# Optimization experiments

Measured on AMD Instinct MI355X. Metric: run time of the kernel, lower is better.

## Reference

```python
import jax, jax.numpy as jnp
import numpy as np

N = 32768          # total nodes
B = 64             # number of graphs (batch.max()+1)
IN_C = 256
OUT_C = 256
NUM_SCALES = 4
NUM_HEADS = 8
BN_EPS = 1e-5


def setup_inputs() -> dict:
    key = jax.random.key(0)
    ks = jax.random.split(key, 10)
    out_s = OUT_C // NUM_SCALES
    x = jax.random.normal(ks[0], (N, IN_C), jnp.float32)
    spectral = jax.random.normal(ks[1], (NUM_SCALES, N, IN_C), jnp.float32)
    batch = jnp.sort(jax.random.randint(ks[2], (N,), 0, B)).astype(jnp.int64)
    # per-scale Linear weights (glorot) and zero biases; stored as [S, in, out_s]
    g = (6.0 / (IN_C + out_s)) ** 0.5
    Ws = jax.random.uniform(ks[3], (NUM_SCALES, IN_C, out_s), jnp.float32, -g, g)
    bs = jnp.zeros((NUM_SCALES, out_s), jnp.float32)
    # MultiheadAttention params (torch layout: in_proj [3E,E], out_proj [E,E])
    s_in = (1.0 / OUT_C) ** 0.5
    W_in = jax.random.uniform(ks[4], (3 * OUT_C, OUT_C), jnp.float32, -s_in, s_in)
    b_in = jnp.zeros((3 * OUT_C,), jnp.float32)
    W_out = jax.random.uniform(ks[5], (OUT_C, OUT_C), jnp.float32, -s_in, s_in)
    b_out = jnp.zeros((OUT_C,), jnp.float32)
    gamma = jnp.ones((OUT_C,), jnp.float32)
    beta = jnp.zeros((OUT_C,), jnp.float32)
    return {"x": x, "spectral": spectral, "Ws": Ws, "bs": bs,
            "W_in": W_in, "b_in": b_in, "W_out": W_out, "b_out": b_out,
            "gamma": gamma, "beta": beta, "batch": batch}


def _forward(x, spectral, Ws, bs, W_in, b_in, W_out, b_out, gamma, beta, batch):
    n, E = x.shape[0], W_out.shape[0]
    # per-scale linear on (x + spectral_feat), concat over scales -> [N, E]
    scale_out = jnp.einsum('sni,sio->sno', x[None] + spectral, Ws) + bs[:, None, :]
    h = jnp.moveaxis(scale_out, 0, 1).reshape(n, E)
    # ragged -> dense padding (batch is sorted segment ids)
    counts = jnp.bincount(batch, length=B)
    max_nodes = int(np.asarray(counts).max())  # data-dependent pad, as in torch
    starts = jnp.concatenate([jnp.zeros((1,), counts.dtype), jnp.cumsum(counts)[:-1]])
    pos = jnp.arange(n) - starts[batch]
    h_pad = jnp.zeros((B, max_nodes, E), h.dtype).at[batch, pos].set(h)
    # MHA over padded graphs (no key-padding mask, matching the source)
    hd = E // NUM_HEADS
    qkv = h_pad @ W_in.T + b_in                       # [B, M, 3E]
    q, k, v = jnp.split(qkv, 3, axis=-1)
    def heads(t):
        return t.reshape(B, max_nodes, NUM_HEADS, hd).transpose(0, 2, 1, 3)
    q, k, v = heads(q) * (hd ** -0.5), heads(k), heads(v)
    attn = jax.nn.softmax(jnp.einsum('bhqd,bhkd->bhqk', q, k), axis=-1)
    ctx = jnp.einsum('bhqk,bhkd->bhqd', attn, v)
    ctx = ctx.transpose(0, 2, 1, 3).reshape(B, max_nodes, E)
    h_att = ctx @ W_out.T + b_out
    # dense -> ragged unpad
    h2 = h_att[batch, pos]                            # [N, E]
    # BatchNorm1d (training-mode batch stats, deterministic) + ReLU; dropout=eval
    mean = h2.mean(axis=0)
    var = h2.var(axis=0)
    hn = (h2 - mean) * jax.lax.rsqrt(var + BN_EPS) * gamma + beta
    return jax.nn.relu(hn)


def reference(x, spectral, Ws, bs, W_in, b_in, W_out, b_out, gamma, beta, batch):
    return _forward(x, spectral, Ws, bs, W_in, b_in, W_out, b_out, gamma, beta, batch)
```

## Files before the change

kernel.cpp:

```cpp
#include <hip/hip_runtime.h>


typedef __attribute__((ext_vector_type(8))) short frag8;
typedef __attribute__((ext_vector_type(4))) float f32x4;
typedef __attribute__((ext_vector_type(8))) unsigned short ushort8;

#define NN 32768
#define NB 64
#define CIN 256
#define COUT 256
#define NHEAD 8
#define HD 32

#define BM 128
#define BK 64
#define LDK 72
#define KT 128

__device__ inline unsigned short f2bf(float f) {
  unsigned u = __builtin_bit_cast(unsigned, f);
  u += 0x7FFFu + ((u >> 16) & 1u);
  return (unsigned short)(u >> 16);
}
__device__ inline unsigned pack2bf(float a, float b) {
  return (unsigned)f2bf(a) | ((unsigned)f2bf(b) << 16);
}

__global__ void k_bounds(const int* __restrict__ batch, int* __restrict__ meta) {
  int i = blockIdx.x * 256 + threadIdx.x;
  if (i >= NN) return;
  int v = batch[i];
  int prev = (i == 0) ? -1 : batch[i - 1];
  for (int bb = prev + 1; bb <= v; ++bb) meta[NB + bb] = i;
}
__global__ void k_meta2(int* __restrict__ meta) {
  __shared__ int mx[NB];
  int b = threadIdx.x;
  int s = meta[NB + b];
  int e = (b == 63) ? NN : meta[NB + b + 1];
  meta[b] = e - s;
  mx[b] = e - s;
  __syncthreads();
  if (b == 0) {
    int m = 0;
    for (int j = 0; j < NB; ++j) m = max(m, mx[j]);
    meta[2 * NB] = m;
  }
}

__global__ void k_prep(const float* __restrict__ Ws, const float* __restrict__ Win,
                       const float* __restrict__ Wout,
                       unsigned short* __restrict__ wst, unsigned short* __restrict__ winb,
                       unsigned short* __restrict__ woutb) {
  int tid = blockIdx.x * 256 + threadIdx.x;
  if (tid < 4 * 64 * 256) {
    int s = tid >> 14, rem = tid & 16383, o = rem >> 8, i = rem & 255;
    wst[tid] = f2bf(Ws[((s * 256) + i) * 64 + o]);
  } else if (tid < 4 * 64 * 256 + 768 * 256) {
    int t2 = tid - 4 * 64 * 256;
    winb[t2] = f2bf(Win[t2]);
  } else if (tid < 4 * 64 * 256 + 768 * 256 + 256 * 256) {
    int t3 = tid - (4 * 64 * 256 + 768 * 256);
    woutb[t3] = f2bf(Wout[t3]);
  }
}

template <int NT>
__device__ inline void mfma_tile(const unsigned short (*As)[LDK],
                                 const unsigned short (*Bs)[LDK],
                                 f32x4 acc[2][NT], int wave, int lane) {
  int m16 = lane & 15, quad = lane >> 4;
#pragma unroll
  for (int kk = 0; kk < 2; ++kk) {
    frag8 a[2], b[NT];
#pragma unroll
    for (int mi = 0; mi < 2; ++mi)
      a[mi] = *(const frag8*)&As[wave * 32 + mi * 16 + m16][kk * 32 + quad * 8];
#pragma unroll
    for (int ni = 0; ni < NT; ++ni)
      b[ni] = *(const frag8*)&Bs[ni * 16 + m16][kk * 32 + quad * 8];
#pragma unroll
    for (int mi = 0; mi < 2; ++mi)
#pragma unroll
      for (int ni = 0; ni < NT; ++ni)
        acc[mi][ni] = __builtin_amdgcn_mfma_f32_16x16x32_bf16(a[mi], b[ni], acc[mi][ni], 0, 0, 0);
  }
}

__device__ inline void stage_B64(const unsigned short* __restrict__ Wt, int c0, int k0,
                                 unsigned short (*Bs)[LDK], int t) {
  int n = t & 63, seg = t >> 6;
  const unsigned short* src = Wt + (size_t)(c0 + n) * 256 + k0 + seg * 16;
  uint4 v0 = *(const uint4*)src;
  uint4 v1 = *(const uint4*)(src + 8);
  *(uint4*)&Bs[n][seg * 16] = v0;
  *(uint4*)&Bs[n][seg * 16 + 8] = v1;
}

__device__ inline void stage_B128(const unsigned short* __restrict__ Wt, int c0, int k0,
                                  unsigned short (*Bs)[LDK], int t) {
  int n = t >> 1, half = t & 1;
  const unsigned short* src = Wt + (size_t)(c0 + n) * 256 + k0 + half * 32;
#pragma unroll
  for (int i = 0; i < 4; ++i) {
    uint4 v = *(const uint4*)(src + i * 8);
    *(uint4*)&Bs[n][half * 32 + i * 8] = v;
  }
}

__device__ inline void stage_A_bf(const unsigned short* __restrict__ A, int lda, int r0, int k0,
                                  unsigned short (*As)[LDK], int t) {
  int r = t >> 1, half = t & 1;
  const unsigned short* src = A + (size_t)(r0 + r) * lda + k0 + half * 32;
#pragma unroll
  for (int i = 0; i < 4; ++i) {
    uint4 v = *(const uint4*)(src + i * 8);
    *(uint4*)&As[r][half * 32 + i * 8] = v;
  }
}

__global__ __launch_bounds__(256) void k_scale(const float* __restrict__ x,
                                               const float* __restrict__ spec,
                                               const unsigned short* __restrict__ wst,
                                               const float* __restrict__ bs,
                                               unsigned short* __restrict__ h) {
  __shared__ unsigned short As[BM][LDK];
  __shared__ unsigned short Bs[64][LDK];
  int t = threadIdx.x, lane = t & 63, wave = t >> 6;
  int r0 = blockIdx.x * BM, s = blockIdx.y;
  f32x4 z = {0.f, 0.f, 0.f, 0.f};
  f32x4 acc[2][4];
#pragma unroll
  for (int mi = 0; mi < 2; ++mi)
#pragma unroll
    for (int ni = 0; ni < 4; ++ni) acc[mi][ni] = z;

  const float* sb = spec + (size_t)s * NN * CIN;
  for (int k0 = 0; k0 < CIN; k0 += BK) {
    {
      int r = t >> 1, half = t & 1;
      const float* xs = x + (size_t)(r0 + r) * CIN + k0 + half * 32;
      const float* ss = sb + (size_t)(r0 + r) * CIN + k0 + half * 32;
#pragma unroll
      for (int i = 0; i < 8; ++i) {
        float4 xv = *(const float4*)(xs + i * 4);
        float4 sv = *(const float4*)(ss + i * 4);
        ushort4 o;
        o.x = f2bf(xv.x + sv.x); o.y = f2bf(xv.y + sv.y);
        o.z = f2bf(xv.z + sv.z); o.w = f2bf(xv.w + sv.w);
        *(ushort4*)&As[r][half * 32 + i * 4] = o;
      }
    }
    stage_B64(wst + (size_t)s * 64 * 256, 0, k0, Bs, t);
    __syncthreads();
    mfma_tile<4>(As, Bs, acc, wave, lane);
    __syncthreads();
  }
  int m16 = lane & 15, quad = lane >> 4;
#pragma unroll
  for (int mi = 0; mi < 2; ++mi)
#pragma unroll
    for (int ni = 0; ni < 4; ++ni) {
      int col = ni * 16 + m16;
      float bias = bs[s * 64 + col];
#pragma unroll
      for (int r = 0; r < 4; ++r) {
        int row = r0 + wave * 32 + mi * 16 + quad * 4 + r;
        h[(size_t)row * COUT + s * 64 + col] = f2bf(acc[mi][ni][r] + bias);
      }
    }
}

template <int LDOUT, bool F32OUT, bool STATS>
__global__ __launch_bounds__(256) void k_lin(const unsigned short* __restrict__ A,
                                             const unsigned short* __restrict__ Wt,
                                             const float* __restrict__ bias,
                                             void* __restrict__ out,
                                             float* __restrict__ sums) {
  __shared__ unsigned short As[BM][LDK];
  __shared__ unsigned short Bs[128][LDK];
  int t = threadIdx.x, lane = t & 63, wave = t >> 6;
  int r0 = blockIdx.x * BM, c0 = blockIdx.y * 128;
  f32x4 z = {0.f, 0.f, 0.f, 0.f};
  f32x4 acc[2][8];
#pragma unroll
  for (int mi = 0; mi < 2; ++mi)
#pragma unroll
    for (int ni = 0; ni < 8; ++ni) acc[mi][ni] = z;

  for (int k0 = 0; k0 < 256; k0 += BK) {
    stage_A_bf(A, 256, r0, k0, As, t);
    stage_B128(Wt, c0, k0, Bs, t);
    __syncthreads();
    mfma_tile<8>(As, Bs, acc, wave, lane);
    __syncthreads();
  }
  int m16 = lane & 15, quad = lane >> 4;
  float cs[8], cs2[8];
#pragma unroll
  for (int ni = 0; ni < 8; ++ni) { cs[ni] = 0.f; cs2[ni] = 0.f; }
#pragma unroll
  for (int mi = 0; mi < 2; ++mi)
#pragma unroll
    for (int ni = 0; ni < 8; ++ni) {
      int col = c0 + ni * 16 + m16;
      float bv = bias[col];
#pragma unroll
      for (int r = 0; r < 4; ++r) {
        int row = r0 + wave * 32 + mi * 16 + quad * 4 + r;
        float v = acc[mi][ni][r] + bv;
        if constexpr (STATS) { cs[ni] += v; cs2[ni] += v * v; }
        if constexpr (F32OUT)
          ((float*)out)[(size_t)row * LDOUT + col] = v;
        else
          ((unsigned short*)out)[(size_t)row * LDOUT + col] = f2bf(v);
      }
    }
  if constexpr (STATS) {
#pragma unroll
    for (int ni = 0; ni < 8; ++ni) {
      float a = cs[ni], b2 = cs2[ni];
      a += __shfl_xor(a, 16); a += __shfl_xor(a, 32);
      b2 += __shfl_xor(b2, 16); b2 += __shfl_xor(b2, 32);
      if (quad == 0) {
        atomicAdd(&sums[c0 + ni * 16 + m16], a);
        atomicAdd(&sums[256 + c0 + ni * 16 + m16], b2);
      }
    }
  }
}

__global__ __launch_bounds__(256) void k_attn_mfma(const unsigned short* __restrict__ qkv,
                                                   const int* __restrict__ meta,
                                                   unsigned short* __restrict__ ctx) {
  int b = blockIdx.x >> 3, head = blockIdx.x & 7;
  int c = meta[b], st = meta[NB + b], M = meta[2 * NB];
  int q0 = blockIdx.y * 128;
  if (q0 >= c) return;

  __shared__ unsigned short Vt[32][KT + 8];

  int t = threadIdx.x, lane = t & 63, wave = t >> 6;
  int m16 = lane & 15, quad = lane >> 4;
  const float SCALE = 0.17677669529663687f;
  float extra = (float)(M - c);

  int qbase = q0 + wave * 32;
  frag8 qf[2];
#pragma unroll
  for (int qg = 0; qg < 2; ++qg) {
    int qrow = qbase + qg * 16 + m16;
    qf[qg] = *(const frag8*)(qkv + (size_t)(st + qrow) * 768 + head * 32 + quad * 8);
  }

  f32x4 zz = {0.f, 0.f, 0.f, 0.f};
  f32x4 O[2][2];
  float lp[2] = {0.f, 0.f};
#pragma unroll
  for (int qg = 0; qg < 2; ++qg) { O[qg][0] = zz; O[qg][1] = zz; }

  int sl0 = m16 + ((quad & 1) << 5);
  int sl1 = sl0 + 16;

  for (int kt = 0; kt < c; kt += KT) {
    {
      int key = t >> 1, dh0 = (t & 1) * 16;
      const unsigned short* vp = qkv + (size_t)(st + kt + key) * 768 + 512 + head * 32 + dh0;
      ushort8 v0 = *(const ushort8*)vp;
      ushort8 v1 = *(const ushort8*)(vp + 8);
#pragma unroll
      for (int i = 0; i < 8; ++i) {
        Vt[dh0 + i][key] = v0[i];
        Vt[dh0 + 8 + i][key] = v1[i];
      }
    }
    __syncthreads();

#pragma unroll
    for (int sub = 0; sub < 4; ++sub) {
      int ks = kt + sub * 32;
      frag8 kf[2];
#pragma unroll
      for (int kh = 0; kh < 2; ++kh) {
        int krow = ks + kh * 16 + m16;
        kf[kh] = *(const frag8*)(qkv + (size_t)(st + krow) * 768 + 256 + head * 32 + quad * 8);
      }
      unsigned pk[2][2][2];
#pragma unroll
      for (int qg = 0; qg < 2; ++qg)
#pragma unroll
        for (int kh = 0; kh < 2; ++kh) {
          f32x4 s = __builtin_amdgcn_mfma_f32_16x16x32_bf16(kf[kh], qf[qg], zz, 0, 0, 0);
          float p[4];
#pragma unroll
          for (int r = 0; r < 4; ++r) {
            int key = ks + kh * 16 + quad * 4 + r;
            float msk = (key < c) ? 1.f : 0.f;
            p[r] = msk * __expf(s[r] * SCALE);
            lp[qg] += p[r];
          }
          pk[qg][kh][0] = pack2bf(p[0], p[1]);
          pk[qg][kh][1] = pack2bf(p[2], p[3]);
        }
      frag8 vf[2];
#pragma unroll
      for (int dh = 0; dh < 2; ++dh)
        vf[dh] = *(const frag8*)&Vt[dh * 16 + m16][sub * 32 + quad * 8];
#pragma unroll
      for (int qg = 0; qg < 2; ++qg) {
        unsigned a0 = __shfl(pk[qg][0][0], sl0), a1 = __shfl(pk[qg][0][1], sl0);
        unsigned a2 = __shfl(pk[qg][0][0], sl1), a3 = __shfl(pk[qg][0][1], sl1);
        unsigned b0 = __shfl(pk[qg][1][0], sl0), b1 = __shfl(pk[qg][1][1], sl0);
        unsigned b2 = __shfl(pk[qg][1][0], sl1), b3 = __shfl(pk[qg][1][1], sl1);
        uint4 pw;
        pw.x = (quad < 2) ? a0 : b0;
        pw.y = (quad < 2) ? a1 : b1;
        pw.z = (quad < 2) ? a2 : b2;
        pw.w = (quad < 2) ? a3 : b3;
        frag8 pf = __builtin_bit_cast(frag8, pw);
#pragma unroll
        for (int dh = 0; dh < 2; ++dh)
          O[qg][dh] = __builtin_amdgcn_mfma_f32_16x16x32_bf16(pf, vf[dh], O[qg][dh], 0, 0, 0);
      }
    }
    __syncthreads();
  }

#pragma unroll
  for (int qg = 0; qg < 2; ++qg) {
    float v = lp[qg];
    v += __shfl_xor(v, 16);
    v += __shfl_xor(v, 32);
    lp[qg] = v;
  }

#pragma unroll
  for (int qg = 0; qg < 2; ++qg)
#pragma unroll
    for (int r = 0; r < 4; ++r) {
      int qrow = qbase + qg * 16 + quad * 4 + r;
      float lsum = __shfl(lp[qg], quad * 4 + r);
      if (qrow < c) {
        float inv = 1.f / (lsum + extra);
        unsigned short* op = ctx + (size_t)(st + qrow) * 256 + head * 32;
        op[m16] = f2bf(O[qg][0][r] * inv);
        op[16 + m16] = f2bf(O[qg][1][r] * inv);
      }
    }
}

__global__ void k_bn_final(const float* __restrict__ sums, const float* __restrict__ gamma,
                           const float* __restrict__ beta, float* __restrict__ bnp) {
  int c = threadIdx.x;
  float mean = sums[c] * (1.0f / NN);
  float var = sums[256 + c] * (1.0f / NN) - mean * mean;
  float sc = rsqrtf(var + 1e-5f) * gamma[c];
  bnp[c] = sc;
  bnp[256 + c] = beta[c] - mean * sc;
}

__global__ __launch_bounds__(256) void k_bn_apply(const float* __restrict__ h,
                                                  const float* __restrict__ bnp,
                                                  float* __restrict__ out) {
  size_t i4 = (size_t)blockIdx.x * 256 + threadIdx.x;
  float4 v = *(const float4*)(h + i4 * 4);
  int c = (int)((i4 * 4) & 255);
  float4 sc = *(const float4*)(bnp + c);
  float4 sh = *(const float4*)(bnp + 256 + c);
  float4 r;
  r.x = fmaxf(v.x * sc.x + sh.x, 0.f);
  r.y = fmaxf(v.y * sc.y + sh.y, 0.f);
  r.z = fmaxf(v.z * sc.z + sh.z, 0.f);
  r.w = fmaxf(v.w * sc.w + sh.w, 0.f);
  *(float4*)(out + i4 * 4) = r;
}

extern "C" void kernel_launch(void* const* d_in, const int* in_sizes, int n_in,
                              void* d_out, int out_size, void* d_ws, size_t ws_size,
                              hipStream_t stream) {
  const float* x      = (const float*)d_in[0];
  const float* spec   = (const float*)d_in[1];
  const float* Ws     = (const float*)d_in[2];
  const float* bs     = (const float*)d_in[3];
  const float* Win    = (const float*)d_in[4];
  const float* b_in   = (const float*)d_in[5];
  const float* Wout   = (const float*)d_in[6];
  const float* b_out  = (const float*)d_in[7];
  const float* gamma  = (const float*)d_in[8];
  const float* beta   = (const float*)d_in[9];
  const int* batch    = (const int*)d_in[10];
  float* out = (float*)d_out;

  char* w = (char*)d_ws;
  size_t off = 0;
  auto alloc = [&](size_t bytes) -> void* {
    off = (off + 255) & ~(size_t)255;
    void* p = w + off; off += bytes; return p;
  };
  int* meta             = (int*)alloc(129 * sizeof(int));
  unsigned short* wst   = (unsigned short*)alloc((size_t)4 * 64 * 256 * 2);
  unsigned short* winb  = (unsigned short*)alloc((size_t)768 * 256 * 2);
  unsigned short* woutb = (unsigned short*)alloc((size_t)256 * 256 * 2);
  float* sums           = (float*)alloc(512 * 4);
  float* bnp            = (float*)alloc(512 * 4);
  unsigned short* h     = (unsigned short*)alloc((size_t)NN * 256 * 2);
  unsigned short* qkv   = (unsigned short*)alloc((size_t)NN * 768 * 2);
  unsigned short* ctx   = (unsigned short*)alloc((size_t)NN * 256 * 2);
  float* hatt           = (float*)alloc((size_t)NN * 256 * 4);

  hipMemsetAsync(sums, 0, 512 * 4, stream);
  k_bounds<<<NN / 256, 256, 0, stream>>>(batch, meta);
  k_meta2<<<1, 64, 0, stream>>>(meta);
  k_prep<<<1280, 256, 0, stream>>>(Ws, Win, Wout, wst, winb, woutb);
  k_scale<<<dim3(NN / BM, 4), 256, 0, stream>>>(x, spec, wst, bs, h);
  k_lin<768, false, false><<<dim3(NN / BM, 6), 256, 0, stream>>>(h, winb, b_in, qkv, nullptr);
  k_attn_mfma<<<dim3(NB * NHEAD, 8), 256, 0, stream>>>(qkv, meta, ctx);
  k_lin<256, true, true><<<dim3(NN / BM, 2), 256, 0, stream>>>(ctx, woutb, b_out, hatt, sums);
  k_bn_final<<<1, 256, 0, stream>>>(sums, gamma, beta, bnp);
  k_bn_apply<<<NN * 256 / 1024, 256, 0, stream>>>(hatt, bnp, out);
}
```

Measured before the change: 440.7 us.

## Merge prep kernels, use 16x16x16 MFMA for PV, bf16 hatt, fold BN finalize

Merges the segment-bounds kernel into the weight-prep kernel and folds the BN finalize step into the BN apply kernel, cutting two launches. The attention PV step now uses the 16x16x16 bf16 MFMA so the probability fragments can be used in place without cross-lane shuffles. Key sub-tiles past the segment end are skipped, and masking is only applied on partial tiles. The out-projection output is stored as bf16 instead of fp32 to halve the intermediate traffic, which costs some precision in the final output, while BN statistics are still accumulated from the projection kernel.

```diff
diff --git a/kernel.cpp b/kernel.cpp
--- a/kernel.cpp
+++ b/kernel.cpp
@@ -2,8 +2,10 @@
 
 
 typedef __attribute__((ext_vector_type(8))) short frag8;
+typedef __attribute__((ext_vector_type(4))) short frag4;
 typedef __attribute__((ext_vector_type(4))) float f32x4;
 typedef __attribute__((ext_vector_type(8))) unsigned short ushort8;
+typedef __attribute__((ext_vector_type(2))) unsigned int uint2e;
 
 #define NN 32768
 #define NB 64
@@ -17,21 +19,44 @@
 #define LDK 72
 #define KT 128
 
+#if __has_builtin(__builtin_amdgcn_mfma_f32_16x16x16bf16_1k)
+#define HAS_MFMA16 1
+#else
+#define HAS_MFMA16 0
+#endif
+
 __device__ inline unsigned short f2bf(float f) {
   unsigned u = __builtin_bit_cast(unsigned, f);
   u += 0x7FFFu + ((u >> 16) & 1u);
   return (unsigned short)(u >> 16);
 }
+__device__ inline float bf2f(unsigned short h) {
+  return __builtin_bit_cast(float, (unsigned)h << 16);
+}
 __device__ inline unsigned pack2bf(float a, float b) {
   return (unsigned)f2bf(a) | ((unsigned)f2bf(b) << 16);
 }
 
-__global__ void k_bounds(const int* __restrict__ batch, int* __restrict__ meta) {
-  int i = blockIdx.x * 256 + threadIdx.x;
-  if (i >= NN) return;
-  int v = batch[i];
-  int prev = (i == 0) ? -1 : batch[i - 1];
-  for (int bb = prev + 1; bb <= v; ++bb) meta[NB + bb] = i;
+__global__ void k_prep(const float* __restrict__ Ws, const float* __restrict__ Win,
+                       const float* __restrict__ Wout, const int* __restrict__ batch,
+                       unsigned short* __restrict__ wst, unsigned short* __restrict__ winb,
+                       unsigned short* __restrict__ woutb, int* __restrict__ meta) {
+  int tid = blockIdx.x * 256 + threadIdx.x;
+  if (tid < NN) {
+    int v = batch[tid];
+    int prev = (tid == 0) ? -1 : batch[tid - 1];
+    for (int bb = prev + 1; bb <= v; ++bb) meta[NB + bb] = tid;
+  }
+  if (tid < 4 * 64 * 256) {
+    int s = tid >> 14, rem = tid & 16383, o = rem >> 8, i = rem & 255;
+    wst[tid] = f2bf(Ws[((s * 256) + i) * 64 + o]);
+  } else if (tid < 4 * 64 * 256 + 768 * 256) {
+    int t2 = tid - 4 * 64 * 256;
+    winb[t2] = f2bf(Win[t2]);
+  } else if (tid < 4 * 64 * 256 + 768 * 256 + 256 * 256) {
+    int t3 = tid - (4 * 64 * 256 + 768 * 256);
+    woutb[t3] = f2bf(Wout[t3]);
+  }
 }
 __global__ void k_meta2(int* __restrict__ meta) {
   __shared__ int mx[NB];
@@ -48,23 +73,6 @@
   }
 }
 
-__global__ void k_prep(const float* __restrict__ Ws, const float* __restrict__ Win,
-                       const float* __restrict__ Wout,
-                       unsigned short* __restrict__ wst, unsigned short* __restrict__ winb,
-                       unsigned short* __restrict__ woutb) {
-  int tid = blockIdx.x * 256 + threadIdx.x;
-  if (tid < 4 * 64 * 256) {
-    int s = tid >> 14, rem = tid & 16383, o = rem >> 8, i = rem & 255;
-    wst[tid] = f2bf(Ws[((s * 256) + i) * 64 + o]);
-  } else if (tid < 4 * 64 * 256 + 768 * 256) {
-    int t2 = tid - 4 * 64 * 256;
-    winb[t2] = f2bf(Win[t2]);
-  } else if (tid < 4 * 64 * 256 + 768 * 256 + 256 * 256) {
-    int t3 = tid - (4 * 64 * 256 + 768 * 256);
-    woutb[t3] = f2bf(Wout[t3]);
-  }
-}
-
 template <int NT>
 __device__ inline void mfma_tile(const unsigned short (*As)[LDK],
                                  const unsigned short (*Bs)[LDK],
@@ -259,8 +267,10 @@
 #pragma unroll
   for (int qg = 0; qg < 2; ++qg) { O[qg][0] = zz; O[qg][1] = zz; }
 
+#if !HAS_MFMA16
   int sl0 = m16 + ((quad & 1) << 5);
   int sl1 = sl0 + 16;
+#endif
 
   for (int kt = 0; kt < c; kt += KT) {
     {
@@ -279,48 +289,71 @@
 #pragma unroll
     for (int sub = 0; sub < 4; ++sub) {
       int ks = kt + sub * 32;
-      frag8 kf[2];
-#pragma unroll
-      for (int kh = 0; kh < 2; ++kh) {
-        int krow = ks + kh * 16 + m16;
-        kf[kh] = *(const frag8*)(qkv + (size_t)(st + krow) * 768 + 256 + head * 32 + quad * 8);
-      }
-      unsigned pk[2][2][2];
-#pragma unroll
-      for (int qg = 0; qg < 2; ++qg)
+      if (ks < c) {
+        bool full = (ks + 32 <= c);
+        frag8 kf[2];
 #pragma unroll
         for (int kh = 0; kh < 2; ++kh) {
-          f32x4 s = __builtin_amdgcn_mfma_f32_16x16x32_bf16(kf[kh], qf[qg], zz, 0, 0, 0);
-          float p[4];
-#pragma unroll
-          for (int r = 0; r < 4; ++r) {
-            int key = ks + kh * 16 + quad * 4 + r;
-            float msk = (key < c) ? 1.f : 0.f;
-            p[r] = msk * __expf(s[r] * SCALE);
-            lp[qg] += p[r];
+          int krow = ks + kh * 16 + m16;
+          kf[kh] = *(const frag8*)(qkv + (size_t)(st + krow) * 768 + 256 + head * 32 + quad * 8);
+        }
+        unsigned pk[2][2][2];
+#pragma unroll
+        for (int qg = 0; qg < 2; ++qg)
+#pragma unroll
+          for (int kh = 0; kh < 2; ++kh) {
+            f32x4 s = __builtin_amdgcn_mfma_f32_16x16x32_bf16(kf[kh], qf[qg], zz, 0, 0, 0);
+            float p[4];
+#pragma unroll
+            for (int r = 0; r < 4; ++r) p[r] = __expf(s[r] * SCALE);
+            if (!full) {
+#pragma unroll
+              for (int r = 0; r < 4; ++r)
+                if (ks + kh * 16 + quad * 4 + r >= c) p[r] = 0.f;
+            }
+            lp[qg] += (p[0] + p[1]) + (p[2] + p[3]);
+            pk[qg][kh][0] = pack2bf(p[0], p[1]);
+            pk[qg][kh][1] = pack2bf(p[2], p[3]);
           }
-          pk[qg][kh][0] = pack2bf(p[0], p[1]);
-          pk[qg][kh][1] = pack2bf(p[2], p[3]);
+#if HAS_MFMA16
+        frag4 vb[2][2];
+#pragma unroll
+        for (int kh = 0; kh < 2; ++kh)
+#pragma unroll
+          for (int dh = 0; dh < 2; ++dh)
+            vb[kh][dh] = *(const frag4*)&Vt[dh * 16 + m16][sub * 32 + kh * 16 + quad * 4];
+#pragma unroll
+        for (int qg = 0; qg < 2; ++qg) {
+          frag4 pa0 = __builtin_bit_cast(frag4, uint2e{pk[qg][0][0], pk[qg][0][1]});
+          frag4 pa1 = __builtin_bit_cast(frag4, uint2e{pk[qg][1][0], pk[qg][1][1]});
+#pragma unroll
+          for (int dh = 0; dh < 2; ++dh) {
+            O[qg][dh] = __builtin_amdgcn_mfma_f32_16x16x16bf16_1k(pa0, vb[0][dh], O[qg][dh], 0, 0, 0);
+            O[qg][dh] = __builtin_amdgcn_mfma_f32_16x16x16bf16_1k(pa1, vb[1][dh], O[qg][dh], 0, 0, 0);
+          }
         }
-      frag8 vf[2];
-#pragma unroll
-      for (int dh = 0; dh < 2; ++dh)
-        vf[dh] = *(const frag8*)&Vt[dh * 16 + m16][sub * 32 + quad * 8];
-#pragma unroll
-      for (int qg = 0; qg < 2; ++qg) {
-        unsigned a0 = __shfl(pk[qg][0][0], sl0), a1 = __shfl(pk[qg][0][1], sl0);
-        unsigned a2 = __shfl(pk[qg][0][0], sl1), a3 = __shfl(pk[qg][0][1], sl1);
-        unsigned b0 = __shfl(pk[qg][1][0], sl0), b1 = __shfl(pk[qg][1][1], sl0);
-        unsigned b2 = __shfl(pk[qg][1][0], sl1), b3 = __shfl(pk[qg][1][1], sl1);
-        uint4 pw;
-        pw.x = (quad < 2) ? a0 : b0;
-        pw.y = (quad < 2) ? a1 : b1;
-        pw.z = (quad < 2) ? a2 : b2;
-        pw.w = (quad < 2) ? a3 : b3;
-        frag8 pf = __builtin_bit_cast(frag8, pw);
+#else
+        frag8 vf[2];
 #pragma unroll
         for (int dh = 0; dh < 2; ++dh)
-          O[qg][dh] = __builtin_amdgcn_mfma_f32_16x16x32_bf16(pf, vf[dh], O[qg][dh], 0, 0, 0);
+          vf[dh] = *(const frag8*)&Vt[dh * 16 + m16][sub * 32 + quad * 8];
+#pragma unroll
+        for (int qg = 0; qg < 2; ++qg) {
+          unsigned a0 = __shfl(pk[qg][0][0], sl0), a1 = __shfl(pk[qg][0][1], sl0);
+          unsigned a2 = __shfl(pk[qg][0][0], sl1), a3 = __shfl(pk[qg][0][1], sl1);
+          unsigned b0 = __shfl(pk[qg][1][0], sl0), b1 = __shfl(pk[qg][1][1], sl0);
+          unsigned b2 = __shfl(pk[qg][1][0], sl1), b3 = __shfl(pk[qg][1][1], sl1);
+          uint4 pw;
+          pw.x = (quad < 2) ? a0 : b0;
+          pw.y = (quad < 2) ? a1 : b1;
+          pw.z = (quad < 2) ? a2 : b2;
+          pw.w = (quad < 2) ? a3 : b3;
+          frag8 pf = __builtin_bit_cast(frag8, pw);
+#pragma unroll
+          for (int dh = 0; dh < 2; ++dh)
+            O[qg][dh] = __builtin_amdgcn_mfma_f32_16x16x32_bf16(pf, vf[dh], O[qg][dh], 0, 0, 0);
+        }
+#endif
       }
     }
     __syncthreads();
@@ -349,30 +382,29 @@
     }
 }
 
-__global__ void k_bn_final(const float* __restrict__ sums, const float* __restrict__ gamma,
-                           const float* __restrict__ beta, float* __restrict__ bnp) {
-  int c = threadIdx.x;
-  float mean = sums[c] * (1.0f / NN);
-  float var = sums[256 + c] * (1.0f / NN) - mean * mean;
-  float sc = rsqrtf(var + 1e-5f) * gamma[c];
-  bnp[c] = sc;
-  bnp[256 + c] = beta[c] - mean * sc;
-}
-
-__global__ __launch_bounds__(256) void k_bn_apply(const float* __restrict__ h,
-                                                  const float* __restrict__ bnp,
+__global__ __launch_bounds__(256) void k_bn_apply(const unsigned short* __restrict__ h,
+                                                  const float* __restrict__ sums,
+                                                  const float* __restrict__ gamma,
+                                                  const float* __restrict__ beta,
                                                   float* __restrict__ out) {
-  size_t i4 = (size_t)blockIdx.x * 256 + threadIdx.x;
-  float4 v = *(const float4*)(h + i4 * 4);
-  int c = (int)((i4 * 4) & 255);
-  float4 sc = *(const float4*)(bnp + c);
-  float4 sh = *(const float4*)(bnp + 256 + c);
-  float4 r;
-  r.x = fmaxf(v.x * sc.x + sh.x, 0.f);
-  r.y = fmaxf(v.y * sc.y + sh.y, 0.f);
-  r.z = fmaxf(v.z * sc.z + sh.z, 0.f);
-  r.w = fmaxf(v.w * sc.w + sh.w, 0.f);
-  *(float4*)(out + i4 * 4) = r;
+  size_t i8 = ((size_t)blockIdx.x * 256 + threadIdx.x) * 8;
+  int c0 = (int)(i8 & 255);
+  ushort8 v = *(const ushort8*)(h + i8);
+  float4 o0, o1;
+  float res[8];
+#pragma unroll
+  for (int i = 0; i < 8; ++i) {
+    int ch = c0 + i;
+    float mean = sums[ch] * (1.0f / NN);
+    float var = sums[256 + ch] * (1.0f / NN) - mean * mean;
+    float sc = rsqrtf(var + 1e-5f) * gamma[ch];
+    float sh = beta[ch] - mean * sc;
+    res[i] = fmaxf(bf2f(v[i]) * sc + sh, 0.f);
+  }
+  o0.x = res[0]; o0.y = res[1]; o0.z = res[2]; o0.w = res[3];
+  o1.x = res[4]; o1.y = res[5]; o1.z = res[6]; o1.w = res[7];
+  *(float4*)(out + i8) = o0;
+  *(float4*)(out + i8 + 4) = o1;
 }
 
 extern "C" void kernel_launch(void* const* d_in, const int* in_sizes, int n_in,
@@ -402,20 +434,17 @@
   unsigned short* winb  = (unsigned short*)alloc((size_t)768 * 256 * 2);
   unsigned short* woutb = (unsigned short*)alloc((size_t)256 * 256 * 2);
   float* sums           = (float*)alloc(512 * 4);
-  float* bnp            = (float*)alloc(512 * 4);
   unsigned short* h     = (unsigned short*)alloc((size_t)NN * 256 * 2);
   unsigned short* qkv   = (unsigned short*)alloc((size_t)NN * 768 * 2);
   unsigned short* ctx   = (unsigned short*)alloc((size_t)NN * 256 * 2);
-  float* hatt           = (float*)alloc((size_t)NN * 256 * 4);
-
-  hipMemsetAsync(sums, 0, 512 * 4, stream);
-  k_bounds<<<NN / 256, 256, 0, stream>>>(batch, meta);
+  unsigned short* hatt  = (unsigned short*)alloc((size_t)NN * 256 * 2);
+
+  (void)hipMemsetAsync(sums, 0, 512 * 4, stream);
+  k_prep<<<1280, 256, 0, stream>>>(Ws, Win, Wout, batch, wst, winb, woutb, meta);
   k_meta2<<<1, 64, 0, stream>>>(meta);
-  k_prep<<<1280, 256, 0, stream>>>(Ws, Win, Wout, wst, winb, woutb);
   k_scale<<<dim3(NN / BM, 4), 256, 0, stream>>>(x, spec, wst, bs, h);
   k_lin<768, false, false><<<dim3(NN / BM, 6), 256, 0, stream>>>(h, winb, b_in, qkv, nullptr);
   k_attn_mfma<<<dim3(NB * NHEAD, 8), 256, 0, stream>>>(qkv, meta, ctx);
-  k_lin<256, true, true><<<dim3(NN / BM, 2), 256, 0, stream>>>(ctx, woutb, b_out, hatt, sums);
-  k_bn_final<<<1, 256, 0, stream>>>(sums, gamma, beta, bnp);
-  k_bn_apply<<<NN * 256 / 1024, 256, 0, stream>>>(hatt, bnp, out);
-}
+  k_lin<256, false, true><<<dim3(NN / BM, 2), 256, 0, stream>>>(ctx, woutb, b_out, hatt, sums);
+  k_bn_apply<<<NN * 256 / 2048, 256, 0, stream>>>(hatt, sums, gamma, beta, out);
+}
```

New measurement: 416.2 us. 1.06x faster.
